# Performance work log

Measured on AMD Instinct MI355X. Metric: run time of the kernel, lower is better.

## Reference

```python
import jax, jax.numpy as jnp
import numpy as np

CONF_W, POS_W, LEN_W, TRIG_W, CONST_W = 1.0, 1.0, 0.1, 1.0, 0.5
FOCAL_THR = 0.1
EPS = 6e-08


def setup_inputs() -> dict:
    key = jax.random.key(0)
    k1, k2, k3, k4, k5 = jax.random.split(key, 5)
    B, C, H, W = 32, 10, 192, 320
    u = jax.random.uniform(k1, (B, H, W), dtype=jnp.float32)
    gt0 = jnp.where(u > 0.95, 1.0, u * 2.0 - 1.0)
    gt_rest = jax.random.normal(k2, (B, C - 1, H, W), dtype=jnp.float32) * 0.5
    gt = jnp.concatenate([gt0[:, None], gt_rest], axis=1)
    # re channel 0: confidence strictly in (0,1) so logs are finite
    re0 = jax.random.uniform(k3, (B, 1, H, W), dtype=jnp.float32, minval=0.05, maxval=0.95)
    re_rest = jax.random.normal(k4, (B, C - 1, H, W), dtype=jnp.float32) * 0.5
    re = jnp.concatenate([re0, re_rest], axis=1)
    return {"re": re, "gt": gt}


def _smooth_l1(d):
    ad = jnp.abs(d)
    return jnp.where(ad < 1.0, 0.5 * d * d, ad - 0.5)


def _forward(re, gt):
    gt0 = gt[:, 0]  # [B,H,W]
    re0 = re[:, 0]
    m0 = gt0 >= 0.0            # confidence mask (above 0)
    mv = gt0 == 1.0            # vehicle mask
    m0f = m0.astype(jnp.float32)
    mvf = mv.astype(jnp.float32)
    nv = mvf.sum()             # number of vehicle pixels (one channel)

    def mse2(rc, gc):
        # mean over two masked channels
        s = sum(((re[:, r] - gt[:, g]) ** 2 * mvf).sum() for r, g in zip(rc, gc))
        return s / (2.0 * nv)

    def sl1_2(rc, gc):
        s = sum((_smooth_l1(re[:, r] - gt[:, g]) * mvf).sum() for r, g in zip(rc, gc))
        return s / (2.0 * nv)

    # focal confidence loss (threshold 0.1) over pixels with gt0 >= 0
    pos = m0f * (gt0 >= FOCAL_THR).astype(jnp.float32)
    neg = m0f * (gt0 < FOCAL_THR).astype(jnp.float32)
    num_pos = pos.sum()
    safe_re = jnp.clip(re0, 1e-6, 1.0 - 1e-6)  # masked-out entries must not NaN
    pos_term = -(pos * (gt0 - re0) ** 2 * jnp.log(safe_re + EPS)).sum()
    neg_term = -(neg * re0 ** 2 * jnp.log(1.0 + EPS - safe_re) * (1.0 - gt0) ** 4).sum()
    focal = jnp.where(num_pos == 0.0, neg_term, (pos_term + neg_term) / num_pos)

    confidence_loss = CONF_W * focal
    pos_loss = POS_W * sl1_2([1, 2], [1, 2])
    length_v1 = LEN_W * sl1_2([3, 6], [3, 6])
    length_v2 = LEN_W * sl1_2([3, 6], [6, 3])
    trig_v1 = TRIG_W * (mse2([4, 7], [4, 7]) + mse2([5, 8], [5, 8]))
    trig_v2 = TRIG_W * (mse2([4, 7], [7, 4]) + mse2([5, 8], [8, 5]))

    const1 = (((1.0 - re[:, 5] ** 2 - re[:, 4] ** 2) ** 2) * mvf).sum() / nv
    const2 = (((1.0 - re[:, 8] ** 2 - re[:, 7] ** 2) ** 2) * mvf).sum() / nv
    const_loss = CONST_W * (const1 + const2)

    height_loss = LEN_W * (_smooth_l1(re[:, 9] - gt[:, 9]) * mvf).sum() / nv

    dimensions_loss = jnp.minimum(length_v1 + trig_v1, length_v2 + trig_v2) + height_loss
    return confidence_loss + pos_loss + dimensions_loss + const_loss


def reference(re, gt):
    return _forward(re, gt)
```

## Files before the change

### kernel.cpp

```cpp
#include <hip/hip_runtime.h>
#include <math.h>

constexpr int B_ = 32, C_ = 10, H_ = 192, W_ = 320;
constexpr int HW_  = H_ * W_;
constexpr int CHW_ = C_ * HW_;
constexpr int NPTS = B_ * HW_;
constexpr int PPT  = 4;
constexpr int TPB  = 128;
constexpr int NTHR = NPTS / PPT;
constexpr int NBLK = NTHR / TPB;

#define NACC 7

typedef float f32x4 __attribute__((ext_vector_type(4)));

__device__ __forceinline__ float sl1f(float d) {
    float ad = fabsf(d);
    return ad < 1.0f ? 0.5f * d * d : ad - 0.5f;
}

__global__ __launch_bounds__(TPB) void loss_main(
    const float* __restrict__ re, const float* __restrict__ gt,
    float* __restrict__ ws)
{
    const int tid = blockIdx.x * TPB + threadIdx.x;
    const int p = tid * PPT;
    const int b = p / HW_;
    const int s = p - b * HW_;
    const float* rp = re + (size_t)b * CHW_ + s;
    const float* gp = gt + (size_t)b * CHW_ + s;

    f32x4 R[10], G[10];
#pragma unroll
    for (int c = 0; c < 10; ++c) {
        R[c] = *(const f32x4*)(rp + c * HW_);
        G[c] = *(const f32x4*)(gp + c * HW_);
    }
    asm volatile(""
        : "+v"(R[0]), "+v"(R[1]), "+v"(R[2]), "+v"(R[3]), "+v"(R[4]),
          "+v"(R[5]), "+v"(R[6]), "+v"(R[7]), "+v"(R[8]), "+v"(R[9]),
          "+v"(G[0]), "+v"(G[1]), "+v"(G[2]), "+v"(G[3]), "+v"(G[4]),
          "+v"(G[5]), "+v"(G[6]), "+v"(G[7]), "+v"(G[8]), "+v"(G[9]));

    float acc[NACC];
#pragma unroll
    for (int i = 0; i < NACC; ++i) acc[i] = 0.0f;

#pragma unroll
    for (int j = 0; j < PPT; ++j) {
        const float g = G[0][j], r = R[0][j];
        const float m = (g == 1.0f) ? 1.0f : 0.0f;
        acc[0] += m;
        const float pos = (g >= 0.1f) ? 1.0f : 0.0f;
        const float neg = ((g >= 0.0f) && (g < 0.1f)) ? 1.0f : 0.0f;
        acc[1] += pos;
        const float safe = fminf(fmaxf(r, 1e-6f), 1.0f - 1e-6f);
        const float larg = (pos != 0.0f) ? (safe + 6e-8f)
                                         : (1.0f + 6e-8f - safe);
        const float lg = logf(larg);
        const float d0 = g - r;
        acc[2] += pos * (d0 * d0) * lg;
        const float omg = 1.0f - g;
        const float omg2 = omg * omg;
        acc[3] += neg * (r * r) * (omg2 * omg2) * lg;

        const float r1 = R[1][j], r2 = R[2][j], r3 = R[3][j], r4v = R[4][j];
        const float r5 = R[5][j], r6 = R[6][j], r7 = R[7][j], r8 = R[8][j],
                    r9 = R[9][j];
        const float g1 = G[1][j], g2 = G[2][j], g3 = G[3][j], g4v = G[4][j];
        const float g5 = G[5][j], g6 = G[6][j], g7 = G[7][j], g8 = G[8][j],
                    g9 = G[9][j];

        const float sp = sl1f(r1 - g1) + sl1f(r2 - g2);
        const float c1 = 1.0f - r5 * r5 - r4v * r4v;
        const float c2 = 1.0f - r8 * r8 - r7 * r7;
        const float sc = c1 * c1 + c2 * c2;
        const float sh = sl1f(r9 - g9);
        acc[4] += m * (0.5f * sp + 0.5f * sc + 0.1f * sh);

        const float d44 = r4v - g4v, d77 = r7 - g7;
        const float d55 = r5 - g5,  d88 = r8 - g8;
        const float t1 = d44 * d44 + d77 * d77 + d55 * d55 + d88 * d88;
        const float l1 = sl1f(r3 - g3) + sl1f(r6 - g6);
        acc[5] += m * (0.05f * l1 + 0.5f * t1);

        const float d47 = r4v - g7, d74 = r7 - g4v;
        const float d58 = r5 - g8,  d85 = r8 - g5;
        const float t2 = d47 * d47 + d74 * d74 + d58 * d58 + d85 * d85;
        const float l2 = sl1f(r3 - g6) + sl1f(r6 - g3);
        acc[6] += m * (0.05f * l2 + 0.5f * t2);
    }

    __shared__ float smem[NACC][2];
    const int lane = threadIdx.x & 63;
    const int wid  = threadIdx.x >> 6;
#pragma unroll
    for (int i = 0; i < NACC; ++i) {
        float v = acc[i];
#pragma unroll
        for (int off = 32; off > 0; off >>= 1) v += __shfl_down(v, off, 64);
        if (lane == 0) smem[i][wid] = v;
    }
    __syncthreads();
    if (threadIdx.x < NACC) {
        const int i = threadIdx.x;
        ws[i * NBLK + blockIdx.x] = smem[i][0] + smem[i][1];
    }
}

__global__ __launch_bounds__(960) void loss_reduce(
    const float* __restrict__ ws, float* __restrict__ out)
{
    float acc[NACC];
#pragma unroll
    for (int i = 0; i < NACC; ++i) acc[i] = 0.0f;

#pragma unroll
    for (int k = 0; k < 4; ++k) {
        const int idx = threadIdx.x + k * 960;
#pragma unroll
        for (int i = 0; i < NACC; ++i)
            acc[i] += ws[i * NBLK + idx];
    }

    __shared__ float smem[NACC][15];
    const int lane = threadIdx.x & 63;
    const int wid  = threadIdx.x >> 6;
#pragma unroll
    for (int i = 0; i < NACC; ++i) {
        float v = acc[i];
#pragma unroll
        for (int off = 32; off > 0; off >>= 1) v += __shfl_down(v, off, 64);
        if (lane == 0) smem[i][wid] = v;
    }
    __syncthreads();

    if (threadIdx.x == 0) {
        float slot[NACC];
#pragma unroll
        for (int i = 0; i < NACC; ++i) {
            float v = 0.0f;
#pragma unroll
            for (int w = 0; w < 15; ++w) v += smem[i][w];
            slot[i] = v;
        }
        const float nv    = slot[0];
        const float npos  = slot[1];
        const float pterm = -slot[2];
        const float nterm = -slot[3];
        const float focal = (npos == 0.0f) ? nterm : (pterm + nterm) / npos;
        out[0] = focal + (slot[4] + fminf(slot[5], slot[6])) / nv;
    }
}

extern "C" void kernel_launch(void* const* d_in, const int* in_sizes, int n_in,
                              void* d_out, int out_size, void* d_ws, size_t ws_size,
                              hipStream_t stream)
{
    const float* re = (const float*)d_in[0];
    const float* gt = (const float*)d_in[1];
    float* ws  = (float*)d_ws;
    float* out = (float*)d_out;

    loss_main<<<NBLK, TPB, 0, stream>>>(re, gt, ws);
    loss_reduce<<<1, 960, 0, stream>>>(ws, out);
}
```

Before: 177.2 us.

## Fuse final reduction into main kernel via last-block atomic counter

Replaces the separate single-block reduce kernel with a last-block-done pattern: each block writes its partials, increments an atomic counter, and the final block reduces all partials and writes the output. It also switches to two points per thread with 256-thread blocks and nontemporal vector loads, and removes the asm register barrier. The aim is to drop a kernel launch and its dependency gap and to make the streaming loads cheaper. In exchange it adds a memset launch, a fence and an atomic per block, and narrower per-thread loads.

```diff
diff --git a/kernel.cpp b/kernel.cpp
--- a/kernel.cpp
+++ b/kernel.cpp
@@ -5,23 +5,24 @@
 constexpr int HW_  = H_ * W_;
 constexpr int CHW_ = C_ * HW_;
 constexpr int NPTS = B_ * HW_;
-constexpr int PPT  = 4;
-constexpr int TPB  = 128;
+constexpr int PPT  = 2;
+constexpr int TPB  = 256;
 constexpr int NTHR = NPTS / PPT;
 constexpr int NBLK = NTHR / TPB;
 
 #define NACC 7
 
-typedef float f32x4 __attribute__((ext_vector_type(4)));
+typedef float f32x2 __attribute__((ext_vector_type(2)));
 
 __device__ __forceinline__ float sl1f(float d) {
     float ad = fabsf(d);
     return ad < 1.0f ? 0.5f * d * d : ad - 0.5f;
 }
 
-__global__ __launch_bounds__(TPB) void loss_main(
+__global__ __launch_bounds__(TPB) void loss_fused(
     const float* __restrict__ re, const float* __restrict__ gt,
-    float* __restrict__ ws)
+    float* __restrict__ ws, unsigned int* __restrict__ cnt,
+    float* __restrict__ out)
 {
     const int tid = blockIdx.x * TPB + threadIdx.x;
     const int p = tid * PPT;
@@ -30,17 +31,12 @@
     const float* rp = re + (size_t)b * CHW_ + s;
     const float* gp = gt + (size_t)b * CHW_ + s;
 
-    f32x4 R[10], G[10];
+    f32x2 R[10], G[10];
 #pragma unroll
     for (int c = 0; c < 10; ++c) {
-        R[c] = *(const f32x4*)(rp + c * HW_);
-        G[c] = *(const f32x4*)(gp + c * HW_);
+        R[c] = __builtin_nontemporal_load((const f32x2*)(rp + c * HW_));
+        G[c] = __builtin_nontemporal_load((const f32x2*)(gp + c * HW_));
     }
-    asm volatile(""
-        : "+v"(R[0]), "+v"(R[1]), "+v"(R[2]), "+v"(R[3]), "+v"(R[4]),
-          "+v"(R[5]), "+v"(R[6]), "+v"(R[7]), "+v"(R[8]), "+v"(R[9]),
-          "+v"(G[0]), "+v"(G[1]), "+v"(G[2]), "+v"(G[3]), "+v"(G[4]),
-          "+v"(G[5]), "+v"(G[6]), "+v"(G[7]), "+v"(G[8]), "+v"(G[9]));
 
     float acc[NACC];
 #pragma unroll
@@ -91,39 +87,7 @@
         acc[6] += m * (0.05f * l2 + 0.5f * t2);
     }
 
-    __shared__ float smem[NACC][2];
-    const int lane = threadIdx.x & 63;
-    const int wid  = threadIdx.x >> 6;
-#pragma unroll
-    for (int i = 0; i < NACC; ++i) {
-        float v = acc[i];
-#pragma unroll
-        for (int off = 32; off > 0; off >>= 1) v += __shfl_down(v, off, 64);
-        if (lane == 0) smem[i][wid] = v;
-    }
-    __syncthreads();
-    if (threadIdx.x < NACC) {
-        const int i = threadIdx.x;
-        ws[i * NBLK + blockIdx.x] = smem[i][0] + smem[i][1];
-    }
-}
-
-__global__ __launch_bounds__(960) void loss_reduce(
-    const float* __restrict__ ws, float* __restrict__ out)
-{
-    float acc[NACC];
-#pragma unroll
-    for (int i = 0; i < NACC; ++i) acc[i] = 0.0f;
-
-#pragma unroll
-    for (int k = 0; k < 4; ++k) {
-        const int idx = threadIdx.x + k * 960;
-#pragma unroll
-        for (int i = 0; i < NACC; ++i)
-            acc[i] += ws[i * NBLK + idx];
-    }
-
-    __shared__ float smem[NACC][15];
+    __shared__ float smem[NACC][4];
     const int lane = threadIdx.x & 63;
     const int wid  = threadIdx.x >> 6;
 #pragma unroll
@@ -135,15 +99,43 @@
     }
     __syncthreads();
 
+    __shared__ int isLast;
+    if (threadIdx.x == 0) {
+#pragma unroll
+        for (int i = 0; i < NACC; ++i)
+            ws[i * NBLK + blockIdx.x] =
+                smem[i][0] + smem[i][1] + smem[i][2] + smem[i][3];
+        __threadfence();
+        isLast = (atomicAdd(cnt, 1u) == (unsigned)(NBLK - 1));
+    }
+    __syncthreads();
+    if (!isLast) return;
+
+    __threadfence();
+    float a2[NACC];
+#pragma unroll
+    for (int i = 0; i < NACC; ++i) a2[i] = 0.0f;
+#pragma unroll
+    for (int k = 0; k < NBLK / TPB; ++k) {
+        const int idx = threadIdx.x + k * TPB;
+#pragma unroll
+        for (int i = 0; i < NACC; ++i)
+            a2[i] += ws[i * NBLK + idx];
+    }
+#pragma unroll
+    for (int i = 0; i < NACC; ++i) {
+        float v = a2[i];
+#pragma unroll
+        for (int off = 32; off > 0; off >>= 1) v += __shfl_down(v, off, 64);
+        if (lane == 0) smem[i][wid] = v;
+    }
+    __syncthreads();
+
     if (threadIdx.x == 0) {
         float slot[NACC];
 #pragma unroll
-        for (int i = 0; i < NACC; ++i) {
-            float v = 0.0f;
-#pragma unroll
-            for (int w = 0; w < 15; ++w) v += smem[i][w];
-            slot[i] = v;
-        }
+        for (int i = 0; i < NACC; ++i)
+            slot[i] = smem[i][0] + smem[i][1] + smem[i][2] + smem[i][3];
         const float nv    = slot[0];
         const float npos  = slot[1];
         const float pterm = -slot[2];
@@ -160,8 +152,9 @@
     const float* re = (const float*)d_in[0];
     const float* gt = (const float*)d_in[1];
     float* ws  = (float*)d_ws;
+    unsigned int* cnt = (unsigned int*)(ws + NACC * NBLK);
     float* out = (float*)d_out;
 
-    loss_main<<<NBLK, TPB, 0, stream>>>(re, gt, ws);
-    loss_reduce<<<1, 960, 0, stream>>>(ws, out);
+    hipMemsetAsync(cnt, 0, sizeof(unsigned int), stream);
+    loss_fused<<<NBLK, TPB, 0, stream>>>(re, gt, ws, cnt, out);
 }
```

New measurement: 332.4 us. +87.6%, slower.
